# Kernel optimization log

Hardware: AMD Instinct MI355X
Metric: run time of the kernel (lower is better)

The kernel has to match this reference:

```python
import jax, jax.numpy as jnp
import numpy as np

B, N, F, D, DEG, LAYERS = 32, 1024, 64, 128, 8, 3
EPS = 1e-5


def _gat(x, src, dst, mask, W, a_s, a_d, b):
    # PyG GATConv (heads=1, concat=True): remove existing self loops (handled by mask),
    # add one self loop per node, per-edge leaky-relu attention, scatter-softmax per target.
    M = x.shape[0]
    h = x @ W                                 # [M, D]
    es = h @ a_s                              # [M] source attention term (x*att_src).sum(-1)
    ed = h @ a_d                              # [M] target attention term
    sl = jnp.arange(M, dtype=src.dtype)
    s = jnp.concatenate([src, sl])
    d = jnp.concatenate([dst, sl])
    m = jnp.concatenate([mask, jnp.ones((M,), bool)])
    logit = jnp.where(m, jax.nn.leaky_relu(es[s] + ed[d], 0.2), -jnp.inf)
    mx = jax.ops.segment_max(logit, d, num_segments=M)  # finite: every node has a self loop
    ex = jnp.where(m, jnp.exp(logit - mx[d]), 0.0)
    den = jax.ops.segment_sum(ex, d, num_segments=M)
    alpha = ex / den[d]
    return jax.ops.segment_sum(alpha[:, None] * h[s], d, num_segments=M) + b


def _dedupe(src, dst, mask, M):
    # coalesce after pooling: drop self loops and duplicate edges (PyG max_pool/pool_edge)
    E = src.shape[0]
    key = src * M + dst
    key = jnp.where(mask, key, M * M + jnp.arange(E, dtype=key.dtype))  # park dead edges on unique keys
    order = jnp.argsort(key)
    sk = key[order]
    first = jnp.concatenate([jnp.ones((1,), bool), sk[1:] != sk[:-1]])
    uniq = jnp.zeros((E,), bool).at[order].set(first)
    return mask & uniq & (src != dst)


def _forward(x, Ws, att_src, att_dst, bias, edge_index, clusters):
    src, dst = edge_index[0], edge_index[1]
    mask = src != dst  # GATConv calls remove_self_loops before adding its own
    Bn = x.shape[0] // clusters[0].shape[0]
    for i in range(len(Ws)):
        x = jax.nn.relu(_gat(x, src, dst, mask, Ws[i], att_src[i], att_dst[i], bias[i]))
        c = clusters[i]
        Ni = c.shape[0]
        No = Ni // 2  # cluster maps are arange(Ni)//2, surjective onto Ni//2
        cl = jnp.tile(c, Bn) + jnp.repeat(jnp.arange(Bn, dtype=c.dtype) * No, Ni)
        x = jax.ops.segment_max(x, cl, num_segments=Bn * No)  # max_pool over clusters
        src, dst = cl[src], cl[dst]
        mask = _dedupe(src, dst, mask, Bn * No)
        mu = jnp.mean(x, axis=0)  # BatchNorm1d(affine=False), training-mode batch stats
        var = jnp.mean((x - mu) ** 2, axis=0)
        x = (x - mu) / jnp.sqrt(var + EPS)
    return x.reshape(Bn, -1)  # [B, final_node * dim_cell]


def setup_inputs() -> dict:
    key = jax.random.key(0)
    ks = jax.random.split(key, 10)
    x = jax.random.normal(ks[0], (B * N, F), jnp.float32)
    # per-graph random edges with per-graph node offsets (graph-major layout)
    src_l = jax.random.randint(ks[1], (B, N * DEG), 0, N)
    dst_l = jax.random.randint(ks[2], (B, N * DEG), 0, N)
    off = (jnp.arange(B) * N)[:, None]
    edge_index = jnp.stack([(src_l + off).reshape(-1), (dst_l + off).reshape(-1)]).astype(jnp.int32)
    c0 = (jnp.arange(N) // 2).astype(jnp.int32)
    c1 = (jnp.arange(N // 2) // 2).astype(jnp.int32)
    c2 = (jnp.arange(N // 4) // 2).astype(jnp.int32)
    W0 = jax.random.normal(ks[3], (F, D), jnp.float32) / np.float32(np.sqrt(F))
    W1 = jax.random.normal(ks[4], (D, D), jnp.float32) / np.float32(np.sqrt(D))
    W2 = jax.random.normal(ks[5], (D, D), jnp.float32) / np.float32(np.sqrt(D))
    att_src = jax.random.normal(ks[6], (LAYERS, D), jnp.float32) / np.float32(np.sqrt(D))
    att_dst = jax.random.normal(ks[7], (LAYERS, D), jnp.float32) / np.float32(np.sqrt(D))
    bias = jnp.zeros((LAYERS, D), jnp.float32)
    return dict(x=x, W0=W0, W1=W1, W2=W2, att_src=att_src, att_dst=att_dst, bias=bias,
                edge_index=edge_index, c0=c0, c1=c1, c2=c2)


def reference(x, W0, W1, W2, att_src, att_dst, bias, edge_index, c0, c1, c2):
    return _forward(x, [W0, W1, W2], att_src, att_dst, bias, edge_index, [c0, c1, c2])
```

## Files before the change

### kernel.cpp

```cpp
#include <hip/hip_runtime.h>

#define E_TOTAL 262144
#define NGRAPH  32
#define EPG     8192
#define EPS_BN  1e-5f
#define MB (1u << 20)
#define KB (1u << 10)

__device__ __forceinline__ float lrelu(float x){ return x > 0.f ? x : 0.2f * x; }

__device__ __forceinline__ int xcd_swz(int b, int n){ return (b & 7) * (n >> 3) + (b >> 3); }

template<int Q>
__device__ __forceinline__ void scan_bins(int* h, int* cnt_g, int* rs_g, int B, int g,
                                          int ebase, int* wsum){
  int t = threadIdx.x, lane = t & 63, w = t >> 6;
  int c[Q]; int s = 0;
  #pragma unroll
  for (int i = 0; i < Q; ++i){ c[i] = h[t * Q + i]; s += c[i]; }
  int v = s;
  #pragma unroll
  for (int o = 1; o < 64; o <<= 1){ int u = __shfl_up(v, o); if (lane >= o) v += u; }
  if (lane == 63) wsum[w] = v;
  __syncthreads();
  if (t == 0){ int run = 0;
    #pragma unroll
    for (int i = 0; i < 4; ++i){ int x = wsum[i]; wsum[i] = run; run += x; } }
  __syncthreads();
  int run = v - s + wsum[w];
  #pragma unroll
  for (int i = 0; i < Q; ++i){
    cnt_g[g * B + t * Q + i] = c[i];
    rs_g [g * B + t * Q + i] = ebase + run;
    h[t * Q + i] = run;
    run += c[i];
  }
  __syncthreads();
}

__global__ __launch_bounds__(256, 2)
void mega1(const float* __restrict__ x0, const float* __restrict__ W0,
           const float* __restrict__ a_s, const float* __restrict__ a_d,
           const int* __restrict__ src0, const int* __restrict__ dst0,
           float* __restrict__ C, float* __restrict__ es, float* __restrict__ ed,
           int* __restrict__ csr1, int* __restrict__ csr2, int* __restrict__ csr3,
           int* __restrict__ rs1, int* __restrict__ rs2, int* __restrict__ rs3,
           int* __restrict__ cnt1, int* __restrict__ cnt2, int* __restrict__ cnt3,
           float* __restrict__ sums_all){
  __shared__ __align__(16) char smem[45072];
  __shared__ int wsum[4];
  int t = threadIdx.x;
  int raw = blockIdx.x;

  if (raw < 96){
    int* bm2 = (int*)smem;
    int* bm3 = bm2 + 8192;
    int* h   = bm3 + 2048;
    int role = raw >> 5, g = raw & 31, ebase = g * EPG;
    if (role == 0 && t < 24) sums_all[g * 24 + t] = 0.f;

    if (role == 0){
      for (int i = t; i < 1024; i += 256) h[i] = 0;
      __syncthreads();
      for (int i = 0; i < 32; ++i){
        int e = ebase + i * 256 + t;
        int sv = src0[e], dv = dst0[e];
        if (sv != dv) atomicAdd(&h[dv & 1023], 1);
      }
      __syncthreads();
      scan_bins<4>(h, cnt1, rs1, 1024, g, ebase, wsum);
      for (int i = 0; i < 32; ++i){
        int e = ebase + i * 256 + t;
        int sv = src0[e], dv = dst0[e];
        if (sv != dv){
          int p = atomicAdd(&h[dv & 1023], 1);
          csr1[ebase + p] = sv;
        }
      }
    } else if (role == 1){
      for (int i = t; i < 8192; i += 256) bm2[i] = 0;
      for (int i = t; i < 512; i += 256) h[i] = 0;
      __syncthreads();
      unsigned int k2m = 0;
      for (int i = 0; i < 32; ++i){
        int e = ebase + i * 256 + t;
        int sv = src0[e], dv = dst0[e];
        if (sv != dv){
          int s2 = (sv >> 1) & 511, d2 = (dv >> 1) & 511;
          if (s2 != d2){
            int key = (s2 << 9) | d2;
            unsigned int bit = 1u << (key & 31);
            unsigned int old = atomicOr((unsigned int*)&bm2[key >> 5], bit);
            if (!(old & bit)){ k2m |= 1u << i; atomicAdd(&h[d2], 1); }
          }
        }
      }
      __syncthreads();
      scan_bins<2>(h, cnt2, rs2, 512, g, ebase, wsum);
      for (int i = 0; i < 32; ++i){
        if ((k2m >> i) & 1u){
          int e = ebase + i * 256 + t;
          int sv = src0[e], dv = dst0[e];
          int p = atomicAdd(&h[(dv >> 1) & 511], 1);
          csr2[ebase + p] = sv >> 1;
        }
      }
    } else {
      for (int i = t; i < 8192; i += 256) bm2[i] = 0;
      for (int i = t; i < 2048; i += 256) bm3[i] = 0;
      for (int i = t; i < 256; i += 256) h[i] = 0;
      __syncthreads();
      unsigned int k3m = 0;
      for (int i = 0; i < 32; ++i){
        int e = ebase + i * 256 + t;
        int sv = src0[e], dv = dst0[e];
        if (sv != dv){
          int s2 = (sv >> 1) & 511, d2 = (dv >> 1) & 511;
          if (s2 != d2){
            int key = (s2 << 9) | d2;
            unsigned int bit = 1u << (key & 31);
            unsigned int old = atomicOr((unsigned int*)&bm2[key >> 5], bit);
            if (!(old & bit)){
              int s3 = (sv >> 2) & 255, d3 = (dv >> 2) & 255;
              if (s3 != d3){
                int key3 = (s3 << 8) | d3;
                unsigned int b3 = 1u << (key3 & 31);
                unsigned int o3 = atomicOr((unsigned int*)&bm3[key3 >> 5], b3);
                if (!(o3 & b3)){ k3m |= 1u << i; atomicAdd(&h[d3], 1); }
              }
            }
          }
        }
      }
      __syncthreads();
      scan_bins<1>(h, cnt3, rs3, 256, g, ebase, wsum);
      for (int i = 0; i < 32; ++i){
        if ((k3m >> i) & 1u){
          int e = ebase + i * 256 + t;
          int sv = src0[e], dv = dst0[e];
          int p = atomicAdd(&h[(dv >> 2) & 255], 1);
          csr3[ebase + p] = sv >> 2;
        }
      }
    }
    return;
  }

  float* Ws   = (float*)smem;
  float* As_t = Ws + 8192;
  int tile = xcd_swz(raw - 96, 1024);
  int row0 = tile * 32;
  int c2 = t & 63, rg = t >> 6;
  float2 acc[8];
  #pragma unroll
  for (int i = 0; i < 8; ++i){ acc[i].x = 0.f; acc[i].y = 0.f; }

  for (int i = t; i < 8192; i += 256) Ws[i] = W0[i];
  #pragma unroll
  for (int it = 0; it < 8; ++it){
    int i = it * 256 + t;
    int r = i >> 6, kk = i & 63;
    As_t[kk * 36 + r] = x0[(size_t)(row0 + r) * 64 + kk];
  }
  __syncthreads();
  #pragma unroll 8
  for (int kk = 0; kk < 64; ++kk){
    float2 w = *(float2*)&Ws[kk * 128 + c2 * 2];
    float4 a0 = *(float4*)&As_t[kk * 36 + rg * 8];
    float4 a1 = *(float4*)&As_t[kk * 36 + rg * 8 + 4];
    acc[0].x = fmaf(a0.x, w.x, acc[0].x); acc[0].y = fmaf(a0.x, w.y, acc[0].y);
    acc[1].x = fmaf(a0.y, w.x, acc[1].x); acc[1].y = fmaf(a0.y, w.y, acc[1].y);
    acc[2].x = fmaf(a0.z, w.x, acc[2].x); acc[2].y = fmaf(a0.z, w.y, acc[2].y);
    acc[3].x = fmaf(a0.w, w.x, acc[3].x); acc[3].y = fmaf(a0.w, w.y, acc[3].y);
    acc[4].x = fmaf(a1.x, w.x, acc[4].x); acc[4].y = fmaf(a1.x, w.y, acc[4].y);
    acc[5].x = fmaf(a1.y, w.x, acc[5].x); acc[5].y = fmaf(a1.y, w.y, acc[5].y);
    acc[6].x = fmaf(a1.z, w.x, acc[6].x); acc[6].y = fmaf(a1.z, w.y, acc[6].y);
    acc[7].x = fmaf(a1.w, w.x, acc[7].x); acc[7].y = fmaf(a1.w, w.y, acc[7].y);
  }
  float2 as2 = ((const float2*)a_s)[c2];
  float2 ad2 = ((const float2*)a_d)[c2];
  float2* C2 = (float2*)C;
  #pragma unroll
  for (int i = 0; i < 8; ++i){
    int r = row0 + rg * 8 + i;
    C2[(size_t)r * 64 + c2] = acc[i];
    float e1 = acc[i].x * as2.x + acc[i].y * as2.y;
    float e2 = acc[i].x * ad2.x + acc[i].y * ad2.y;
    #pragma unroll
    for (int o = 32; o; o >>= 1){ e1 += __shfl_xor(e1, o); e2 += __shfl_xor(e2, o); }
    if (c2 == 0){ es[r] = e1; ed[r] = e2; }
  }
}

__global__ __launch_bounds__(256)
void gemm_attn128(const float* __restrict__ A, const float* __restrict__ W,
                  const float* __restrict__ bnsums, float invM,
                  const float* __restrict__ a_s, const float* __restrict__ a_d,
                  float* __restrict__ C, float* __restrict__ es, float* __restrict__ ed){
  __shared__ float Ws[64 * 128];
  __shared__ float As_t[64 * 36];
  __shared__ float bnmu[128], bnrs[128];
  int t = threadIdx.x;
  if (t < 128){
    float mu = bnsums[t] * invM;
    float var = bnsums[128 + t] * invM - mu * mu;
    bnmu[t] = mu; bnrs[t] = rsqrtf(var + EPS_BN);
  }
  int bid = xcd_swz(blockIdx.x, gridDim.x);
  int row0 = bid * 32;
  int c2 = t & 63, rg = t >> 6;
  float2 acc[8];
  #pragma unroll
  for (int i = 0; i < 8; ++i){ acc[i].x = 0.f; acc[i].y = 0.f; }

  for (int k0 = 0; k0 < 128; k0 += 64){
    __syncthreads();
    for (int i = t; i < 64 * 128; i += 256)
      Ws[i] = W[(size_t)(k0 + (i >> 7)) * 128 + (i & 127)];
    #pragma unroll
    for (int it = 0; it < 8; ++it){
      int i = it * 256 + t;
      int r = i >> 6, kk = i & 63;
      float v = A[(size_t)(row0 + r) * 128 + k0 + kk];
      v = (v - bnmu[k0 + kk]) * bnrs[k0 + kk];
      As_t[kk * 36 + r] = v;
    }
    __syncthreads();
    #pragma unroll 8
    for (int kk = 0; kk < 64; ++kk){
      float2 w = *(float2*)&Ws[kk * 128 + c2 * 2];
      float4 a0 = *(float4*)&As_t[kk * 36 + rg * 8];
      float4 a1 = *(float4*)&As_t[kk * 36 + rg * 8 + 4];
      acc[0].x = fmaf(a0.x, w.x, acc[0].x); acc[0].y = fmaf(a0.x, w.y, acc[0].y);
      acc[1].x = fmaf(a0.y, w.x, acc[1].x); acc[1].y = fmaf(a0.y, w.y, acc[1].y);
      acc[2].x = fmaf(a0.z, w.x, acc[2].x); acc[2].y = fmaf(a0.z, w.y, acc[2].y);
      acc[3].x = fmaf(a0.w, w.x, acc[3].x); acc[3].y = fmaf(a0.w, w.y, acc[3].y);
      acc[4].x = fmaf(a1.x, w.x, acc[4].x); acc[4].y = fmaf(a1.x, w.y, acc[4].y);
      acc[5].x = fmaf(a1.y, w.x, acc[5].x); acc[5].y = fmaf(a1.y, w.y, acc[5].y);
      acc[6].x = fmaf(a1.z, w.x, acc[6].x); acc[6].y = fmaf(a1.z, w.y, acc[6].y);
      acc[7].x = fmaf(a1.w, w.x, acc[7].x); acc[7].y = fmaf(a1.w, w.y, acc[7].y);
    }
  }
  float2 as2 = ((const float2*)a_s)[c2];
  float2 ad2 = ((const float2*)a_d)[c2];
  float2* C2 = (float2*)C;
  #pragma unroll
  for (int i = 0; i < 8; ++i){
    int r = row0 + rg * 8 + i;
    C2[(size_t)r * 64 + c2] = acc[i];
    float e1 = acc[i].x * as2.x + acc[i].y * as2.y;
    float e2 = acc[i].x * ad2.x + acc[i].y * ad2.y;
    #pragma unroll
    for (int o = 32; o; o >>= 1){ e1 += __shfl_xor(e1, o); e2 += __shfl_xor(e2, o); }
    if (c2 == 0){ es[r] = e1; ed[r] = e2; }
  }
}

__global__ void gat_pool(const float* __restrict__ h, const float* __restrict__ es,
                         const float* __restrict__ ed, const int* __restrict__ csr_src,
                         const int* __restrict__ row_start, const int* __restrict__ row_cnt,
                         const float* __restrict__ bias, float* __restrict__ xout, int M){
  __shared__ float2 osh[4][64];
  int lane = threadIdx.x & 63;
  int wave = threadIdx.x >> 6;
  int bid = xcd_swz(blockIdx.x, gridDim.x);
  int n = bid * 4 + wave;
  int start = row_start[n];
  int cnt   = row_cnt[n];
  float edn = ed[n];
  float selfl = lrelu(es[n] + edn);

  float m_l = -1e30f, d_l = 0.f;
  int   s_c = 0; float l_c = 0.f;
  for (int c0 = 0; c0 < cnt; c0 += 64){
    int j = c0 + lane;
    if (j < cnt){
      int s = csr_src[start + j];
      float l = lrelu(es[s] + edn);
      if (c0 == 0){ s_c = s; l_c = l; }
      float mn = fmaxf(m_l, l);
      d_l = d_l * __expf(m_l - mn) + __expf(l - mn);
      m_l = mn;
    }
  }
  #pragma unroll
  for (int o = 32; o; o >>= 1){
    float m2 = __shfl_xor(m_l, o), d2 = __shfl_xor(d_l, o);
    float mn = fmaxf(m_l, m2);
    d_l = d_l * __expf(m_l - mn) + d2 * __expf(m2 - mn);
    m_l = mn;
  }
  float mf  = fmaxf(m_l, selfl);
  float den = d_l * __expf(m_l - mf) + __expf(selfl - mf);

  const float2* h2 = (const float2*)h;
  float sw = __expf(selfl - mf);
  float2 hv = h2[(size_t)n * 64 + lane];
  float2 acc; acc.x = sw * hv.x; acc.y = sw * hv.y;
  for (int c0 = 0; c0 < cnt; c0 += 64){
    int j = c0 + lane;
    int s_j; float w_j;
    if (c0 == 0){
      s_j = s_c;
      w_j = (lane < cnt) ? __expf(l_c - mf) : 0.f;
    } else {
      s_j = 0; w_j = 0.f;
      if (j < cnt){
        s_j = csr_src[start + j];
        w_j = __expf(lrelu(es[s_j] + edn) - mf);
      }
    }
    int rem = min(64, cnt - c0);
    int k = 0;
    for (; k + 8 <= rem; k += 8){
      int ss[8]; float ww[8]; float2 hh[8];
      #pragma unroll
      for (int i = 0; i < 8; ++i){ ss[i] = __shfl(s_j, k + i); ww[i] = __shfl(w_j, k + i); }
      #pragma unroll
      for (int i = 0; i < 8; ++i){ hh[i] = h2[(size_t)ss[i] * 64 + lane]; }
      #pragma unroll
      for (int i = 0; i < 8; ++i){
        acc.x = fmaf(ww[i], hh[i].x, acc.x);
        acc.y = fmaf(ww[i], hh[i].y, acc.y);
      }
    }
    for (; k < rem; ++k){
      int s = __shfl(s_j, k); float w = __shfl(w_j, k);
      float2 hh = h2[(size_t)s * 64 + lane];
      acc.x = fmaf(w, hh.x, acc.x);
      acc.y = fmaf(w, hh.y, acc.y);
    }
  }
  float inv = 1.f / den;
  float2 bv = ((const float2*)bias)[lane];
  float2 o2;
  o2.x = fmaxf(acc.x * inv + bv.x, 0.f);
  o2.y = fmaxf(acc.y * inv + bv.y, 0.f);
  osh[wave][lane] = o2;
  __syncthreads();
  if (wave < 2){
    float2 a = osh[2 * wave][lane], b = osh[2 * wave + 1][lane];
    float2 p; p.x = fmaxf(a.x, b.x); p.y = fmaxf(a.y, b.y);
    ((float2*)xout)[(size_t)(bid * 2 + wave) * 64 + lane] = p;
  }
}

__global__ void bn_stats(const float* __restrict__ x, float* __restrict__ sums, int M){
  __shared__ float s1[256], s2[256];
  int c = threadIdx.x & 127, half = threadIdx.x >> 7;
  float a = 0.f, b = 0.f;
  for (int r = blockIdx.x * 2 + half; r < M; r += 256){
    float v = x[(size_t)r * 128 + c];
    a += v; b += v * v;
  }
  s1[threadIdx.x] = a; s2[threadIdx.x] = b;
  __syncthreads();
  if (threadIdx.x < 128){
    atomicAdd(&sums[c],       s1[threadIdx.x] + s1[threadIdx.x + 128]);
    atomicAdd(&sums[128 + c], s2[threadIdx.x] + s2[threadIdx.x + 128]);
  }
}

__global__ void bn_norm(const float* __restrict__ in, const float* __restrict__ sums,
                        float* __restrict__ out, int M){
  int idx = blockIdx.x * blockDim.x + threadIdx.x;
  if (idx >= M * 128) return;
  int c = idx & 127;
  float mu  = sums[c] / (float)M;
  float var = sums[128 + c] / (float)M - mu * mu;
  out[idx] = (in[idx] - mu) * rsqrtf(var + EPS_BN);
}

extern "C" void kernel_launch(void* const* d_in, const int* in_sizes, int n_in,
                              void* d_out, int out_size, void* d_ws, size_t ws_size,
                              hipStream_t stream){
  const float* x0   = (const float*)d_in[0];
  const float* W0   = (const float*)d_in[1];
  const float* W1   = (const float*)d_in[2];
  const float* W2   = (const float*)d_in[3];
  const float* attS = (const float*)d_in[4];
  const float* attD = (const float*)d_in[5];
  const float* bias = (const float*)d_in[6];
  const int*   src0 = (const int*)d_in[7];
  const int*   dst0 = src0 + E_TOTAL;
  float* out = (float*)d_out;

  char* ws = (char*)d_ws;
  float* Hbuf   = (float*)(ws);
  float* Xbuf   = (float*)(ws + 16 * MB);
  int*   csr1   = (int*)  (ws + 24 * MB);
  int*   csr2   = (int*)  (ws + 25 * MB);
  int*   csr3   = (int*)  (ws + 26 * MB);
  float* es     = (float*)(ws + 27 * MB);
  float* ed     = (float*)(ws + 27 * MB + 128 * KB);
  int*   rs1    = (int*)  (ws + 27 * MB + 256 * KB);
  int*   rs2    = (int*)  (ws + 27 * MB + 384 * KB);
  int*   rs3    = (int*)  (ws + 27 * MB + 448 * KB);
  int*   cnt1   = (int*)  (ws + 27 * MB + 480 * KB);
  int*   cnt2   = (int*)  (ws + 27 * MB + 608 * KB);
  int*   cnt3   = (int*)  (ws + 27 * MB + 672 * KB);
  float* sums   = (float*)(ws + 27 * MB + 704 * KB);
  float* sums0 = sums, *sums1 = sums + 256, *sums2 = sums + 512;

  mega1<<<1120, 256, 0, stream>>>(x0, W0, attS, attD, src0, dst0, Hbuf, es, ed,
                                  csr1, csr2, csr3, rs1, rs2, rs3, cnt1, cnt2, cnt3,
                                  sums);

  gat_pool<<<8192, 256, 0, stream>>>(Hbuf, es, ed, csr1, rs1, cnt1, bias, Xbuf, 32768);

  bn_stats<<<128, 256, 0, stream>>>(Xbuf, sums0, 16384);
  gemm_attn128<<<512, 256, 0, stream>>>(Xbuf, W1, sums0, 1.f / 16384.f,
                                        attS + 128, attD + 128, Hbuf, es, ed);
  gat_pool<<<4096, 256, 0, stream>>>(Hbuf, es, ed, csr2, rs2, cnt2, bias + 128, Xbuf, 16384);

  bn_stats<<<128, 256, 0, stream>>>(Xbuf, sums1, 8192);
  gemm_attn128<<<256, 256, 0, stream>>>(Xbuf, W2, sums1, 1.f / 8192.f,
                                        attS + 256, attD + 256, Hbuf, es, ed);
  gat_pool<<<2048, 256, 0, stream>>>(Hbuf, es, ed, csr3, rs3, cnt3, bias + 256, Xbuf, 8192);

  bn_stats<<<128, 256, 0, stream>>>(Xbuf, sums2, 4096);
  bn_norm<<<2048, 256, 0, stream>>>(Xbuf, sums2, out, 4096);
}
```

Before: 227.4 us.

## Fuse batch-norm statistics into gat_pool epilogue via sharded atomic partials

Removes the three separate bn_stats launches. Each gat_pool block now atomically adds its pooled outputs and their squares into one of 64 sharded partial-sum slots, which are zeroed up front by mega1. The consumers (gemm_attn128 and bn_norm) reduce the 64 partials in their prologue, and bn_norm becomes a grid-stride kernel with per-block shared mean and rstd. This trades three launches and a re-read of Xbuf for extra atomics and syncs in gat_pool and a redundant 64-way partial reduction in every consumer block.

```diff
diff --git a/kernel.cpp b/kernel.cpp
--- a/kernel.cpp
+++ b/kernel.cpp
@@ -46,7 +46,7 @@
            int* __restrict__ csr1, int* __restrict__ csr2, int* __restrict__ csr3,
            int* __restrict__ rs1, int* __restrict__ rs2, int* __restrict__ rs3,
            int* __restrict__ cnt1, int* __restrict__ cnt2, int* __restrict__ cnt3,
-           float* __restrict__ sums_all){
+           float* __restrict__ partials_all){
   __shared__ __align__(16) char smem[45072];
   __shared__ int wsum[4];
   int t = threadIdx.x;
@@ -57,9 +57,9 @@
     int* bm3 = bm2 + 8192;
     int* h   = bm3 + 2048;
     int role = raw >> 5, g = raw & 31, ebase = g * EPG;
-    if (role == 0 && t < 24) sums_all[g * 24 + t] = 0.f;
 
     if (role == 0){
+      for (int i = g * 256 + t; i < 3 * 64 * 256; i += 8192) partials_all[i] = 0.f;
       for (int i = t; i < 1024; i += 256) h[i] = 0;
       __syncthreads();
       for (int i = 0; i < 32; ++i){
@@ -194,16 +194,24 @@
 
 __global__ __launch_bounds__(256)
 void gemm_attn128(const float* __restrict__ A, const float* __restrict__ W,
-                  const float* __restrict__ bnsums, float invM,
+                  const float* __restrict__ partials, float invM,
                   const float* __restrict__ a_s, const float* __restrict__ a_d,
                   float* __restrict__ C, float* __restrict__ es, float* __restrict__ ed){
   __shared__ float Ws[64 * 128];
   __shared__ float As_t[64 * 36];
+  __shared__ float red[256];
   __shared__ float bnmu[128], bnrs[128];
   int t = threadIdx.x;
+  {
+    float s = 0.f;
+    #pragma unroll
+    for (int k = 0; k < 64; ++k) s += partials[(k << 8) + t];
+    red[t] = s;
+  }
+  __syncthreads();
   if (t < 128){
-    float mu = bnsums[t] * invM;
-    float var = bnsums[128 + t] * invM - mu * mu;
+    float mu = red[t] * invM;
+    float var = red[128 + t] * invM - mu * mu;
     bnmu[t] = mu; bnrs[t] = rsqrtf(var + EPS_BN);
   }
   int bid = xcd_swz(blockIdx.x, gridDim.x);
@@ -259,7 +267,8 @@
 __global__ void gat_pool(const float* __restrict__ h, const float* __restrict__ es,
                          const float* __restrict__ ed, const int* __restrict__ csr_src,
                          const int* __restrict__ row_start, const int* __restrict__ row_cnt,
-                         const float* __restrict__ bias, float* __restrict__ xout, int M){
+                         const float* __restrict__ bias, float* __restrict__ xout,
+                         float* __restrict__ partials, int M){
   __shared__ float2 osh[4][64];
   int lane = threadIdx.x & 63;
   int wave = threadIdx.x >> 6;
@@ -338,37 +347,51 @@
   o2.y = fmaxf(acc.y * inv + bv.y, 0.f);
   osh[wave][lane] = o2;
   __syncthreads();
+  float2 p;
   if (wave < 2){
     float2 a = osh[2 * wave][lane], b = osh[2 * wave + 1][lane];
-    float2 p; p.x = fmaxf(a.x, b.x); p.y = fmaxf(a.y, b.y);
+    p.x = fmaxf(a.x, b.x); p.y = fmaxf(a.y, b.y);
     ((float2*)xout)[(size_t)(bid * 2 + wave) * 64 + lane] = p;
   }
-}
-
-__global__ void bn_stats(const float* __restrict__ x, float* __restrict__ sums, int M){
-  __shared__ float s1[256], s2[256];
-  int c = threadIdx.x & 127, half = threadIdx.x >> 7;
-  float a = 0.f, b = 0.f;
-  for (int r = blockIdx.x * 2 + half; r < M; r += 256){
-    float v = x[(size_t)r * 128 + c];
-    a += v; b += v * v;
-  }
-  s1[threadIdx.x] = a; s2[threadIdx.x] = b;
-  __syncthreads();
-  if (threadIdx.x < 128){
-    atomicAdd(&sums[c],       s1[threadIdx.x] + s1[threadIdx.x + 128]);
-    atomicAdd(&sums[128 + c], s2[threadIdx.x] + s2[threadIdx.x + 128]);
-  }
-}
-
-__global__ void bn_norm(const float* __restrict__ in, const float* __restrict__ sums,
-                        float* __restrict__ out, int M){
-  int idx = blockIdx.x * blockDim.x + threadIdx.x;
-  if (idx >= M * 128) return;
-  int c = idx & 127;
-  float mu  = sums[c] / (float)M;
-  float var = sums[128 + c] / (float)M - mu * mu;
-  out[idx] = (in[idx] - mu) * rsqrtf(var + EPS_BN);
+  __syncthreads();
+  if (wave < 2) osh[wave][lane] = p;
+  __syncthreads();
+  float* part = partials + ((bid & 63) << 8);
+  if (wave == 0){
+    float2 a = osh[0][lane], b = osh[1][lane];
+    atomicAdd(&part[2 * lane],     a.x + b.x);
+    atomicAdd(&part[2 * lane + 1], a.y + b.y);
+  } else if (wave == 1){
+    float2 a = osh[0][lane], b = osh[1][lane];
+    atomicAdd(&part[128 + 2 * lane],     a.x * a.x + b.x * b.x);
+    atomicAdd(&part[128 + 2 * lane + 1], a.y * a.y + b.y * b.y);
+  }
+}
+
+__global__ __launch_bounds__(256)
+void bn_norm(const float* __restrict__ in, const float* __restrict__ partials,
+             float* __restrict__ out, int M){
+  __shared__ float red[256];
+  __shared__ float mu_s[128], rs_s[128];
+  int t = threadIdx.x;
+  {
+    float s = 0.f;
+    #pragma unroll
+    for (int k = 0; k < 64; ++k) s += partials[(k << 8) + t];
+    red[t] = s;
+  }
+  __syncthreads();
+  if (t < 128){
+    float mu = red[t] / (float)M;
+    float var = red[128 + t] / (float)M - mu * mu;
+    mu_s[t] = mu; rs_s[t] = rsqrtf(var + EPS_BN);
+  }
+  __syncthreads();
+  int total = M * 128;
+  for (int idx = blockIdx.x * 256 + t; idx < total; idx += gridDim.x * 256){
+    int c = idx & 127;
+    out[idx] = (in[idx] - mu_s[c]) * rs_s[c];
+  }
 }
 
 extern "C" void kernel_launch(void* const* d_in, const int* in_sizes, int n_in,
@@ -399,25 +422,25 @@
   int*   cnt1   = (int*)  (ws + 27 * MB + 480 * KB);
   int*   cnt2   = (int*)  (ws + 27 * MB + 608 * KB);
   int*   cnt3   = (int*)  (ws + 27 * MB + 672 * KB);
-  float* sums   = (float*)(ws + 27 * MB + 704 * KB);
-  float* sums0 = sums, *sums1 = sums + 256, *sums2 = sums + 512;
+  float* parts  = (float*)(ws + 27 * MB + 704 * KB);
+  float* parts0 = parts, *parts1 = parts + 64 * 256, *parts2 = parts + 2 * 64 * 256;
 
   mega1<<<1120, 256, 0, stream>>>(x0, W0, attS, attD, src0, dst0, Hbuf, es, ed,
                                   csr1, csr2, csr3, rs1, rs2, rs3, cnt1, cnt2, cnt3,
-                                  sums);
-
-  gat_pool<<<8192, 256, 0, stream>>>(Hbuf, es, ed, csr1, rs1, cnt1, bias, Xbuf, 32768);
-
-  bn_stats<<<128, 256, 0, stream>>>(Xbuf, sums0, 16384);
-  gemm_attn128<<<512, 256, 0, stream>>>(Xbuf, W1, sums0, 1.f / 16384.f,
+                                  parts);
+
+  gat_pool<<<8192, 256, 0, stream>>>(Hbuf, es, ed, csr1, rs1, cnt1, bias, Xbuf,
+                                     parts0, 32768);
+
+  gemm_attn128<<<512, 256, 0, stream>>>(Xbuf, W1, parts0, 1.f / 16384.f,
                                         attS + 128, attD + 128, Hbuf, es, ed);
-  gat_pool<<<4096, 256, 0, stream>>>(Hbuf, es, ed, csr2, rs2, cnt2, bias + 128, Xbuf, 16384);
-
-  bn_stats<<<128, 256, 0, stream>>>(Xbuf, sums1, 8192);
-  gemm_attn128<<<256, 256, 0, stream>>>(Xbuf, W2, sums1, 1.f / 8192.f,
+  gat_pool<<<4096, 256, 0, stream>>>(Hbuf, es, ed, csr2, rs2, cnt2, bias + 128, Xbuf,
+                                     parts1, 16384);
+
+  gemm_attn128<<<256, 256, 0, stream>>>(Xbuf, W2, parts1, 1.f / 8192.f,
                                         attS + 256, attD + 256, Hbuf, es, ed);
-  gat_pool<<<2048, 256, 0, stream>>>(Hbuf, es, ed, csr3, rs3, cnt3, bias + 256, Xbuf, 8192);
-
-  bn_stats<<<128, 256, 0, stream>>>(Xbuf, sums2, 4096);
-  bn_norm<<<2048, 256, 0, stream>>>(Xbuf, sums2, out, 4096);
-}
+  gat_pool<<<2048, 256, 0, stream>>>(Hbuf, es, ed, csr3, rs3, cnt3, bias + 256, Xbuf,
+                                     parts2, 8192);
+
+  bn_norm<<<512, 256, 0, stream>>>(Xbuf, parts2, out, 4096);
+}
```

After: 203.6 us. -10.5%, faster.
